# Kernel optimization log

Measured on AMD Instinct MI355X. Metric: run time of the kernel, lower is better.

The kernel has to match this reference:

```python
import jax, jax.numpy as jnp
import numpy as np

B, S, E = 8, 2048, 512
H = 8          # attention heads (and also number of sampling points)
P = 8          # deformable sampling points per token
Dh = E // H


def setup_inputs() -> dict:
    key = jax.random.key(0)
    ks = jax.random.split(key, 9)
    scale = 0.02
    return {
        "q": jax.random.normal(ks[0], (B, S, E), jnp.float32),
        "k": jax.random.normal(ks[1], (B, S, E), jnp.float32),
        "v": jax.random.normal(ks[2], (B, S, E), jnp.float32),
        "offset_w": jax.random.normal(ks[3], (2 * P, E), jnp.float32) * scale,
        "offset_b": jnp.zeros((2 * P,), jnp.float32),
        "in_proj_w": jax.random.normal(ks[4], (3 * E, E), jnp.float32) * scale,
        "in_proj_b": jnp.zeros((3 * E,), jnp.float32),
        "out_w": jax.random.normal(ks[5], (E, E), jnp.float32) * scale,
        "out_b": jnp.zeros((E,), jnp.float32),
    }


def reference(q, k, v, offset_w, offset_b, in_proj_w, in_proj_b, out_w, out_b):
    b, s, e = q.shape
    # learned offsets: [B,S,P,2]; only component 0 is used as a temporal offset
    offsets = (q @ offset_w.T + offset_b).reshape(b, s, P, 2)
    t = jnp.arange(s, dtype=q.dtype)[None, :, None]                # [1,S,1]
    # index = clamp(int(t + off0), 0, S-1); python int() truncates toward zero
    idx = jnp.clip(jnp.trunc(t + offsets[..., 0]).astype(jnp.int32), 0, s - 1)  # [B,S,P]
    # gather sampled K/V: [B,S,P,E]
    sk = jnp.take_along_axis(k[:, :, None, :], idx[..., None], axis=1)
    sv = jnp.take_along_axis(v[:, :, None, :], idx[..., None], axis=1)

    # nn.MultiheadAttention with query len 1 per token, kv len P, batch = B*S
    wq, wk, wv = in_proj_w[:e], in_proj_w[e:2 * e], in_proj_w[2 * e:]
    bq, bk, bv = in_proj_b[:e], in_proj_b[e:2 * e], in_proj_b[2 * e:]
    n = b * s
    qp = (q.reshape(n, e) @ wq.T + bq).reshape(n, H, Dh)            # [N,H,Dh]
    kp = (sk.reshape(n, P, e) @ wk.T + bk).reshape(n, P, H, Dh)     # [N,P,H,Dh]
    vp = (sv.reshape(n, P, e) @ wv.T + bv).reshape(n, P, H, Dh)
    scores = jnp.einsum('nhd,nphd->nhp', qp, kp) / np.sqrt(Dh)      # [N,H,P]
    attn = jax.nn.softmax(scores, axis=-1)
    ctx = jnp.einsum('nhp,nphd->nhd', attn, vp).reshape(n, e)       # [N,E]
    out = ctx @ out_w.T + out_b
    return out.reshape(b, s, e)
```

## Files before the change

### kernel.cpp

```cpp
#include <hip/hip_runtime.h>

#define S_LEN 2048
#define E_DIM 512
#define NTOK  16384
#define QBLK  1024
#define CVTBLK 4096

typedef __bf16 bf16x8_t __attribute__((ext_vector_type(8)));
typedef __bf16 bf16x4_t __attribute__((ext_vector_type(4)));
typedef float f32x4_t __attribute__((ext_vector_type(4)));
typedef unsigned short u16x8_t __attribute__((ext_vector_type(8)));
typedef unsigned short u16x4_t __attribute__((ext_vector_type(4)));

__device__ __forceinline__ float bf2f(unsigned short h) {
  return __uint_as_float(((unsigned)h) << 16);
}
__device__ __forceinline__ u16x8_t cvt8n(float4 a, float4 b) {
  bf16x8_t t;
  t[0] = (__bf16)a.x; t[1] = (__bf16)a.y; t[2] = (__bf16)a.z; t[3] = (__bf16)a.w;
  t[4] = (__bf16)b.x; t[5] = (__bf16)b.y; t[6] = (__bf16)b.z; t[7] = (__bf16)b.w;
  union { bf16x8_t h; u16x8_t u; } cv; cv.h = t; return cv.u;
}
__device__ __forceinline__ u16x4_t cvt4n(float4 a) {
  bf16x4_t t;
  t[0] = (__bf16)a.x; t[1] = (__bf16)a.y; t[2] = (__bf16)a.z; t[3] = (__bf16)a.w;
  union { bf16x4_t h; u16x4_t u; } cv; cv.h = t; return cv.u;
}
__device__ __forceinline__ void gload16(const void* g, void* l) {
  __builtin_amdgcn_global_load_lds(
      (const __attribute__((address_space(1))) unsigned int*)g,
      (__attribute__((address_space(3))) unsigned int*)l, 16, 0, 0);
}

__global__ __launch_bounds__(256)
void prepass_kernel(const float* __restrict__ q, const float* __restrict__ k,
                    const float* __restrict__ v, const float* __restrict__ ipw,
                    const float* __restrict__ outw, const float* __restrict__ ow,
                    const float* __restrict__ ob, int* __restrict__ idx,
                    unsigned short* __restrict__ Qbf, unsigned short* __restrict__ Kb,
                    unsigned short* __restrict__ Vb, unsigned short* __restrict__ Wb,
                    unsigned short* __restrict__ OWb)
{
  const int bid = blockIdx.x;
  if (bid >= QBLK) {
    const size_t NG = 4456448;
    const size_t gstride = (size_t)CVTBLK * 256;
    for (size_t g = (size_t)(bid - QBLK) * 256 + threadIdx.x; g < NG; g += gstride) {
      const float* src; unsigned short* dst; size_t e;
      if (g < 2097152)      { src = k;    dst = Kb;  e = g * 4; }
      else if (g < 4194304) { src = v;    dst = Vb;  e = (g - 2097152) * 4; }
      else if (g < 4390912) { src = ipw;  dst = Wb;  e = (g - 4194304) * 4; }
      else                  { src = outw; dst = OWb; e = (g - 4390912) * 4; }
      *(u16x4_t*)(dst + e) = cvt4n(*(const float4*)(src + e));
    }
    return;
  }

  __shared__ float wl[8][548];
  __shared__ float ql[4][548];

  {
    const int r  = threadIdx.x >> 5;
    const int e0 = (threadIdx.x & 31) * 16;
    const float* src = ow + (size_t)(2 * r) * E_DIM + e0;
    #pragma unroll
    for (int c = 0; c < 4; ++c) {
      const int e = e0 + c * 4;
      *(float4*)&wl[r][(e >> 6) * 68 + (e & 63)] = *(const float4*)(src + c * 4);
    }
  }
  __syncthreads();

  const int w    = threadIdx.x >> 6;
  const int lane = threadIdx.x & 63;
  const int j    = lane >> 3;
  const int p    = lane & 7;

  for (int it = 0; it < 4; ++it) {
    const int n = bid * 16 + w * 4 + it;
    const float* qr = q + (size_t)n * E_DIM + lane * 8;
    const float4 q0 = *(const float4*)qr;
    const float4 q1 = *(const float4*)(qr + 4);
    *(u16x8_t*)(Qbf + (size_t)n * E_DIM + lane * 8) = cvt8n(q0, q1);
    const int e  = lane * 8;
    const int ph = (e >> 6) * 68 + (e & 63);
    *(float4*)&ql[w][ph]     = q0;
    *(float4*)&ql[w][ph + 4] = q1;

    float acc = 0.f;
    #pragma unroll
    for (int i4 = 0; i4 < 16; ++i4) {
      const float4 qv = *(const float4*)&ql[w][j * 68 + i4 * 4];
      const float4 wv = *(const float4*)&wl[p][j * 68 + i4 * 4];
      acc = fmaf(qv.x, wv.x, acc); acc = fmaf(qv.y, wv.y, acc);
      acc = fmaf(qv.z, wv.z, acc); acc = fmaf(qv.w, wv.w, acc);
    }
    acc += __shfl_xor(acc, 8, 64);
    acc += __shfl_xor(acc, 16, 64);
    acc += __shfl_xor(acc, 32, 64);
    if (lane < 8) {
      const float val = (float)(n & (S_LEN - 1)) + acc + ob[2 * lane];
      int id = (int)truncf(val);
      id = id < 0 ? 0 : (id > S_LEN - 1 ? S_LEN - 1 : id);
      idx[n * 8 + lane] = id;
    }
    __syncthreads();
  }
}

__global__ __launch_bounds__(256, 2)
void gemm3_kernel(const unsigned short* __restrict__ Qbf, const unsigned short* __restrict__ Kbf,
                  const unsigned short* __restrict__ Vbf, const unsigned short* __restrict__ W,
                  const float* __restrict__ bias, unsigned short* __restrict__ Cout)
{
  __shared__ __align__(16) unsigned short sA[2][128 * 64];
  __shared__ __align__(16) unsigned short sB[2][128 * 64];

  const int t    = threadIdx.x;
  const int lane = t & 63;
  const int wid  = t >> 6;
  const int wm   = wid >> 1;
  const int wn   = wid & 1;
  const size_t m0 = (size_t)blockIdx.x * 128;
  const size_t n0 = (size_t)blockIdx.y * 128;

  const int srow0  = wid * 32;
  const int schunk = (lane & 7) ^ (lane >> 3);
  const size_t aoff = (m0 + srow0 + (lane >> 3)) * E_DIM + schunk * 8;
  const unsigned short* gA[3] = { Qbf + aoff, Kbf + aoff, Vbf + aoff };
  const unsigned short* gB = W + (n0 + srow0 + (lane >> 3)) * E_DIM + schunk * 8;

#define STAGE(buf, z_, k0) do { \
    _Pragma("unroll") \
    for (int i_ = 0; i_ < 4; ++i_) { \
      gload16(gA[z_] + (size_t)(i_ * 8) * E_DIM + (k0), &sA[buf][(srow0 + i_ * 8) * 64]); \
      gload16(gB + (size_t)(z_) * E_DIM * E_DIM + (size_t)(i_ * 8) * E_DIM + (k0), \
              &sB[buf][(srow0 + i_ * 8) * 64]); \
    } } while (0)

  f32x4_t acc[4][4];
  #pragma unroll
  for (int i = 0; i < 4; ++i)
    #pragma unroll
    for (int j = 0; j < 4; ++j)
      acc[i][j] = (f32x4_t){0.f, 0.f, 0.f, 0.f};

  STAGE(0, 0, 0);
  int cur = 0;
  const int fr = lane & 15;
  const int ck0 = lane >> 4;

  for (int it = 0; it < 24; ++it) {
    const int z  = it >> 3;
    const int kt = it & 7;
    __syncthreads();
    if (it < 23) {
      const int nz = (it + 1) >> 3;
      const int nk = (it + 1) & 7;
      STAGE(cur ^ 1, nz, nk * 64);
    }
    #pragma unroll
    for (int kk = 0; kk < 64; kk += 32) {
      const int ckb = (kk >> 3) + ck0;
      bf16x8_t af[4], bfv[4];
      #pragma unroll
      for (int i = 0; i < 4; ++i) {
        const int ra = wm * 64 + i * 16 + fr;
        af[i] = *(const bf16x8_t*)&sA[cur][ra * 64 + ((ckb ^ (ra & 7)) << 3)];
      }
      #pragma unroll
      for (int j = 0; j < 4; ++j) {
        const int rb = wn * 64 + j * 16 + fr;
        bfv[j] = *(const bf16x8_t*)&sB[cur][rb * 64 + ((ckb ^ (rb & 7)) << 3)];
      }
      #pragma unroll
      for (int i = 0; i < 4; ++i)
        #pragma unroll
        for (int j = 0; j < 4; ++j)
          acc[i][j] = __builtin_amdgcn_mfma_f32_16x16x32_bf16(af[i], bfv[j], acc[i][j], 0, 0, 0);
    }
    if (kt == 7) {
      unsigned short* Cb = Cout + (size_t)z * NTOK * E_DIM;
      #pragma unroll
      for (int i = 0; i < 4; ++i) {
        const int row = (int)m0 + wm * 64 + i * 16 + (lane >> 4) * 4;
        #pragma unroll
        for (int j = 0; j < 4; ++j) {
          const int col = (int)n0 + wn * 64 + j * 16 + fr;
          const float bv = bias[z * E_DIM + col];
          #pragma unroll
          for (int r = 0; r < 4; ++r) {
            Cb[(size_t)(row + r) * E_DIM + col] =
                __builtin_bit_cast(unsigned short, (__bf16)(acc[i][j][r] + bv));
            acc[i][j][r] = 0.f;
          }
        }
      }
    }
    cur ^= 1;
  }
#undef STAGE
}

__global__ __launch_bounds__(256, 2)
void gemm_kernel(const unsigned short* __restrict__ A, const unsigned short* __restrict__ W,
                 const float* __restrict__ bias, float* __restrict__ Cf)
{
  __shared__ __align__(16) unsigned short sA[2][128 * 64];
  __shared__ __align__(16) unsigned short sB[2][128 * 64];

  const int t    = threadIdx.x;
  const int lane = t & 63;
  const int wid  = t >> 6;
  const int wm   = wid >> 1;
  const int wn   = wid & 1;
  const size_t m0 = (size_t)blockIdx.x * 128;
  const size_t n0 = (size_t)blockIdx.y * 128;

  const int srow0  = wid * 32;
  const int schunk = (lane & 7) ^ (lane >> 3);
  const unsigned short* gA = A + (m0 + srow0 + (lane >> 3)) * E_DIM + schunk * 8;
  const unsigned short* gB = W + (n0 + srow0 + (lane >> 3)) * E_DIM + schunk * 8;

#define STAGE(buf, k0) do { \
    _Pragma("unroll") \
    for (int i_ = 0; i_ < 4; ++i_) { \
      gload16(gA + (size_t)(i_ * 8) * E_DIM + (k0), &sA[buf][(srow0 + i_ * 8) * 64]); \
      gload16(gB + (size_t)(i_ * 8) * E_DIM + (k0), &sB[buf][(srow0 + i_ * 8) * 64]); \
    } } while (0)

  f32x4_t acc[4][4];
  #pragma unroll
  for (int i = 0; i < 4; ++i)
    #pragma unroll
    for (int j = 0; j < 4; ++j)
      acc[i][j] = (f32x4_t){0.f, 0.f, 0.f, 0.f};

  STAGE(0, 0);
  int cur = 0;
  const int fr = lane & 15;
  const int ck0 = lane >> 4;

  for (int kt = 0; kt < 8; ++kt) {
    __syncthreads();
    if (kt < 7) STAGE(cur ^ 1, (kt + 1) * 64);
    #pragma unroll
    for (int kk = 0; kk < 64; kk += 32) {
      const int ckb = (kk >> 3) + ck0;
      bf16x8_t af[4], bfv[4];
      #pragma unroll
      for (int i = 0; i < 4; ++i) {
        const int ra = wm * 64 + i * 16 + fr;
        af[i] = *(const bf16x8_t*)&sA[cur][ra * 64 + ((ckb ^ (ra & 7)) << 3)];
      }
      #pragma unroll
      for (int j = 0; j < 4; ++j) {
        const int rb = wn * 64 + j * 16 + fr;
        bfv[j] = *(const bf16x8_t*)&sB[cur][rb * 64 + ((ckb ^ (rb & 7)) << 3)];
      }
      #pragma unroll
      for (int i = 0; i < 4; ++i)
        #pragma unroll
        for (int j = 0; j < 4; ++j)
          acc[i][j] = __builtin_amdgcn_mfma_f32_16x16x32_bf16(af[i], bfv[j], acc[i][j], 0, 0, 0);
    }
    cur ^= 1;
  }
#undef STAGE

  #pragma unroll
  for (int i = 0; i < 4; ++i) {
    const int row = (int)m0 + wm * 64 + i * 16 + (lane >> 4) * 4;
    #pragma unroll
    for (int j = 0; j < 4; ++j) {
      const int col = (int)n0 + wn * 64 + j * 16 + fr;
      const float bv = bias[col];
      #pragma unroll
      for (int r = 0; r < 4; ++r)
        Cf[(size_t)(row + r) * E_DIM + col] = acc[i][j][r] + bv;
    }
  }
}

__global__ __launch_bounds__(256)
void attn_kernel(const unsigned short* __restrict__ Qp, const unsigned short* __restrict__ Kp,
                 const unsigned short* __restrict__ Vp, const int* __restrict__ idx,
                 unsigned short* __restrict__ ctx)
{
  const int wid  = threadIdx.x >> 6;
  const int lane = threadIdx.x & 63;
  const int n = blockIdx.x * 4 + wid;
  const int b = n >> 11;
  const int h = lane >> 3;
  const int p = lane & 7;

  const int id = idx[n * 8 + p];
  const size_t krow = ((size_t)(b << 11) + id) * E_DIM + h * 64;
  const unsigned short* qb = Qp + (size_t)n * E_DIM + h * 64;

  float sc = 0.f;
  #pragma unroll
  for (int j = 0; j < 8; ++j) {
    u16x8_t qv = *(const u16x8_t*)(qb + j * 8);
    u16x8_t kv = *(const u16x8_t*)(Kp + krow + j * 8);
    #pragma unroll
    for (int e = 0; e < 8; ++e) sc += bf2f(qv[e]) * bf2f(kv[e]);
  }
  sc *= 0.125f;

  float m = sc;
  m = fmaxf(m, __shfl_xor(m, 1, 64));
  m = fmaxf(m, __shfl_xor(m, 2, 64));
  m = fmaxf(m, __shfl_xor(m, 4, 64));
  const float ex = __expf(sc - m);
  float dsum = ex;
  dsum += __shfl_xor(dsum, 1, 64);
  dsum += __shfl_xor(dsum, 2, 64);
  dsum += __shfl_xor(dsum, 4, 64);
  const float attn = ex / dsum;

  const int d0 = p * 8;
  float cacc[8];
  #pragma unroll
  for (int j = 0; j < 8; ++j) cacc[j] = 0.f;
  #pragma unroll
  for (int pp = 0; pp < 8; ++pp) {
    const float ap = __shfl(attn, (lane & 56) + pp, 64);
    const int  idp = __shfl(id,   (lane & 56) + pp, 64);
    const unsigned short* vb = Vp + ((size_t)(b << 11) + idp) * E_DIM + h * 64 + d0;
    u16x8_t vv = *(const u16x8_t*)vb;
    #pragma unroll
    for (int j = 0; j < 8; ++j) cacc[j] += ap * bf2f(vv[j]);
  }
  u16x8_t cc;
  #pragma unroll
  for (int j = 0; j < 8; ++j) cc[j] = __builtin_bit_cast(unsigned short, (__bf16)cacc[j]);
  *(u16x8_t*)(ctx + (size_t)n * E_DIM + h * 64 + d0) = cc;
}

extern "C" void kernel_launch(void* const* d_in, const int* in_sizes, int n_in,
                              void* d_out, int out_size, void* d_ws, size_t ws_size,
                              hipStream_t stream) {
  const float* q        = (const float*)d_in[0];
  const float* k        = (const float*)d_in[1];
  const float* v        = (const float*)d_in[2];
  const float* offset_w = (const float*)d_in[3];
  const float* offset_b = (const float*)d_in[4];
  const float* in_proj_w = (const float*)d_in[5];
  const float* in_proj_b = (const float*)d_in[6];
  const float* out_w    = (const float*)d_in[7];
  const float* out_b    = (const float*)d_in[8];

  char* ws = (char*)d_ws;
  unsigned short* Qbf = (unsigned short*)ws;
  unsigned short* Kbf = Qbf + (size_t)NTOK * E_DIM;
  unsigned short* Vbf = Kbf + (size_t)NTOK * E_DIM;
  unsigned short* Wb  = Vbf + (size_t)NTOK * E_DIM;
  unsigned short* OWb = Wb + (size_t)3 * E_DIM * E_DIM;
  unsigned short* Qp  = OWb + (size_t)E_DIM * E_DIM;
  unsigned short* Kp  = Qp + (size_t)NTOK * E_DIM;
  unsigned short* Vp  = Kp + (size_t)NTOK * E_DIM;
  int* idxb = (int*)(Vp + (size_t)NTOK * E_DIM);
  unsigned short* ctxb = Qbf;

  prepass_kernel<<<QBLK + CVTBLK, 256, 0, stream>>>(q, k, v, in_proj_w, out_w, offset_w,
                                                    offset_b, idxb, Qbf, Kbf, Vbf, Wb, OWb);
  gemm3_kernel<<<dim3(NTOK / 128, E_DIM / 128), 256, 0, stream>>>(
      Qbf, Kbf, Vbf, Wb, in_proj_b, Qp);
  attn_kernel<<<NTOK / 4, 256, 0, stream>>>(Qp, Kp, Vp, idxb, ctxb);
  gemm_kernel<<<dim3(NTOK / 128, E_DIM / 128), 256, 0, stream>>>(
      ctxb, OWb, out_b, (float*)d_out);
}
```

Before: 102.4 us.

## Enlarge projection GEMM tile and deepen pipeline to triple-buffered LDS

The QKV projection GEMM now uses 512-thread blocks with a 256x128 output tile, so each B tile is reused across more rows. The LDS pipeline goes from double to triple buffering, using explicit vmcnt waits and raw barriers so loads stay in flight two stages ahead. MFMA sections also run at raised wave priority. The cost is more LDS (about 144KB) and one block per CU, which lowers occupancy and relies on hand-tuned waitcnt values being correct.

After: 107.0 us. 1.04x slower.

```diff
diff --git a/kernel.cpp b/kernel.cpp
--- a/kernel.cpp
+++ b/kernel.cpp
@@ -58,7 +58,6 @@
 
   __shared__ float wl[8][548];
   __shared__ float ql[4][548];
-
   {
     const int r  = threadIdx.x >> 5;
     const int e0 = (threadIdx.x & 31) * 16;
@@ -108,35 +107,40 @@
   }
 }
 
-__global__ __launch_bounds__(256, 2)
-void gemm3_kernel(const unsigned short* __restrict__ Qbf, const unsigned short* __restrict__ Kbf,
-                  const unsigned short* __restrict__ Vbf, const unsigned short* __restrict__ W,
+__global__ __launch_bounds__(512, 1)
+void gemm3_kernel(const unsigned short* __restrict__ Abase,
+                  const unsigned short* __restrict__ W,
                   const float* __restrict__ bias, unsigned short* __restrict__ Cout)
 {
-  __shared__ __align__(16) unsigned short sA[2][128 * 64];
-  __shared__ __align__(16) unsigned short sB[2][128 * 64];
+  __shared__ __align__(16) unsigned short sA[3][256 * 64];
+  __shared__ __align__(16) unsigned short sB[3][128 * 64];
 
   const int t    = threadIdx.x;
   const int lane = t & 63;
   const int wid  = t >> 6;
   const int wm   = wid >> 1;
   const int wn   = wid & 1;
-  const size_t m0 = (size_t)blockIdx.x * 128;
+  const size_t m0 = (size_t)blockIdx.x * 256;
   const size_t n0 = (size_t)blockIdx.y * 128;
 
-  const int srow0  = wid * 32;
+  const int sArow0 = wid * 32;
+  const int sBrow0 = wid * 16;
   const int schunk = (lane & 7) ^ (lane >> 3);
-  const size_t aoff = (m0 + srow0 + (lane >> 3)) * E_DIM + schunk * 8;
-  const unsigned short* gA[3] = { Qbf + aoff, Kbf + aoff, Vbf + aoff };
-  const unsigned short* gB = W + (n0 + srow0 + (lane >> 3)) * E_DIM + schunk * 8;
-
-#define STAGE(buf, z_, k0) do { \
+  const size_t aoff = (m0 + sArow0 + (lane >> 3)) * E_DIM + schunk * 8;
+  const size_t boff = (n0 + sBrow0 + (lane >> 3)) * E_DIM + schunk * 8;
+
+#define STAGE(sl, it_) do { \
+    const int z_ = (it_) >> 3; \
+    const int k0_ = ((it_) & 7) * 64; \
+    const unsigned short* gA_ = Abase + (size_t)z_ * NTOK * E_DIM + aoff; \
+    const unsigned short* gB_ = W + (size_t)z_ * E_DIM * E_DIM + boff; \
     _Pragma("unroll") \
-    for (int i_ = 0; i_ < 4; ++i_) { \
-      gload16(gA[z_] + (size_t)(i_ * 8) * E_DIM + (k0), &sA[buf][(srow0 + i_ * 8) * 64]); \
-      gload16(gB + (size_t)(z_) * E_DIM * E_DIM + (size_t)(i_ * 8) * E_DIM + (k0), \
-              &sB[buf][(srow0 + i_ * 8) * 64]); \
-    } } while (0)
+    for (int i_ = 0; i_ < 4; ++i_) \
+      gload16(gA_ + (size_t)(i_ * 8) * E_DIM + k0_, &sA[sl][(sArow0 + i_ * 8) * 64]); \
+    _Pragma("unroll") \
+    for (int i_ = 0; i_ < 2; ++i_) \
+      gload16(gB_ + (size_t)(i_ * 8) * E_DIM + k0_, &sB[sl][(sBrow0 + i_ * 8) * 64]); \
+  } while (0)
 
   f32x4_t acc[4][4];
   #pragma unroll
@@ -145,20 +149,19 @@
     for (int j = 0; j < 4; ++j)
       acc[i][j] = (f32x4_t){0.f, 0.f, 0.f, 0.f};
 
-  STAGE(0, 0, 0);
-  int cur = 0;
+  STAGE(0, 0);
+  STAGE(1, 1);
   const int fr = lane & 15;
   const int ck0 = lane >> 4;
 
   for (int it = 0; it < 24; ++it) {
-    const int z  = it >> 3;
-    const int kt = it & 7;
-    __syncthreads();
-    if (it < 23) {
-      const int nz = (it + 1) >> 3;
-      const int nk = (it + 1) & 7;
-      STAGE(cur ^ 1, nz, nk * 64);
-    }
+    if (it < 23) asm volatile("s_waitcnt vmcnt(6)" ::: "memory");
+    else         asm volatile("s_waitcnt vmcnt(0)" ::: "memory");
+    __builtin_amdgcn_sched_barrier(0);
+    __builtin_amdgcn_s_barrier();
+    __builtin_amdgcn_sched_barrier(0);
+    if (it + 2 < 24) STAGE((it + 2) % 3, it + 2);
+    const int sl = it % 3;
     #pragma unroll
     for (int kk = 0; kk < 64; kk += 32) {
       const int ckb = (kk >> 3) + ck0;
@@ -166,20 +169,23 @@
       #pragma unroll
       for (int i = 0; i < 4; ++i) {
         const int ra = wm * 64 + i * 16 + fr;
-        af[i] = *(const bf16x8_t*)&sA[cur][ra * 64 + ((ckb ^ (ra & 7)) << 3)];
+        af[i] = *(const bf16x8_t*)&sA[sl][ra * 64 + ((ckb ^ (ra & 7)) << 3)];
       }
       #pragma unroll
       for (int j = 0; j < 4; ++j) {
         const int rb = wn * 64 + j * 16 + fr;
-        bfv[j] = *(const bf16x8_t*)&sB[cur][rb * 64 + ((ckb ^ (rb & 7)) << 3)];
-      }
+        bfv[j] = *(const bf16x8_t*)&sB[sl][rb * 64 + ((ckb ^ (rb & 7)) << 3)];
+      }
+      __builtin_amdgcn_s_setprio(1);
       #pragma unroll
       for (int i = 0; i < 4; ++i)
         #pragma unroll
         for (int j = 0; j < 4; ++j)
           acc[i][j] = __builtin_amdgcn_mfma_f32_16x16x32_bf16(af[i], bfv[j], acc[i][j], 0, 0, 0);
-    }
-    if (kt == 7) {
+      __builtin_amdgcn_s_setprio(0);
+    }
+    if ((it & 7) == 7) {
+      const int z = it >> 3;
       unsigned short* Cb = Cout + (size_t)z * NTOK * E_DIM;
       #pragma unroll
       for (int i = 0; i < 4; ++i) {
@@ -197,7 +203,6 @@
         }
       }
     }
-    cur ^= 1;
   }
 #undef STAGE
 }
@@ -365,8 +370,7 @@
 
   prepass_kernel<<<QBLK + CVTBLK, 256, 0, stream>>>(q, k, v, in_proj_w, out_w, offset_w,
                                                     offset_b, idxb, Qbf, Kbf, Vbf, Wb, OWb);
-  gemm3_kernel<<<dim3(NTOK / 128, E_DIM / 128), 256, 0, stream>>>(
-      Qbf, Kbf, Vbf, Wb, in_proj_b, Qp);
+  gemm3_kernel<<<dim3(NTOK / 256, E_DIM / 128), 512, 0, stream>>>(Qbf, Wb, in_proj_b, Qp);
   attn_kernel<<<NTOK / 4, 256, 0, stream>>>(Qp, Kp, Vp, idxb, ctxb);
   gemm_kernel<<<dim3(NTOK / 128, E_DIM / 128), 256, 0, stream>>>(
       ctxb, OWb, out_b, (float*)d_out);
```
